# Performance work log

Measured on AMD Instinct MI355X. Metric: run time of the kernel, lower is better.

The kernel has to match this reference:

```python
import jax, jax.numpy as jnp
import numpy as np

# Model dims (match init_kwargs)
IN, H, N, W, OUT, R = 128, 512, 2048, 64, 128, 4
EPS = 1e-8


def setup_inputs() -> dict:
    key = jax.random.key(0)
    ks = jax.random.split(key, 10)
    T, B = 128, 64
    ctrl_in = IN + R * W
    s = lambda n: 1.0 / np.sqrt(n)
    return {
        "x_seq": jax.random.normal(ks[0], (T, B, IN), jnp.float32),
        "Wih": jax.random.normal(ks[1], (4 * H, ctrl_in), jnp.float32) * s(ctrl_in),
        "Whh": jax.random.normal(ks[2], (4 * H, H), jnp.float32) * s(H),
        "bih": jnp.zeros((4 * H,), jnp.float32),
        "bhh": jnp.zeros((4 * H,), jnp.float32),
        "Wout": jax.random.normal(ks[3], (OUT, H), jnp.float32) * s(H),
        "bout": jnp.zeros((OUT,), jnp.float32),
        "Wkey": jax.random.normal(ks[4], ((R + 1) * W, H), jnp.float32) * s(H),
        "bkey": jnp.zeros(((R + 1) * W,), jnp.float32),
        "alpha": jnp.float32(0.5),
        "gamma": jnp.float32(0.95),
    }


def _forward(x_seq, Wih, Whh, bih, bhh, Wout, bout, Wkey, bkey, alpha, gamma):
    T, B, _ = x_seq.shape
    h = jnp.zeros((B, H), x_seq.dtype)
    c = jnp.zeros((B, H), x_seq.dtype)
    usage = jnp.zeros((B, N), x_seq.dtype)
    read_w = jnp.zeros((B, R, N), x_seq.dtype)
    read_vec = jnp.zeros((B, R * W), x_seq.dtype)
    M = jnp.full((B, N, W), 1e-6, x_seq.dtype)  # memory reset to small const

    def step(carry, x_t):
        h, c, M, usage, read_w, read_vec = carry
        # --- LSTM controller ---
        x = jnp.concatenate([x_t, read_vec], axis=1)
        gates = x @ Wih.T + h @ Whh.T + bih + bhh  # (B, 4H)
        i, f, g, o = jnp.split(gates, 4, axis=1)
        c_new = jax.nn.sigmoid(f) * c + jax.nn.sigmoid(i) * jnp.tanh(g)
        h_new = jax.nn.sigmoid(o) * jnp.tanh(c_new)
        out = h_new @ Wout.T + bout  # (B, OUT)
        keys = (h_new @ Wkey.T + bkey).reshape(B, R + 1, W)
        read_keys = keys[:, :R]       # (B, R, W)
        write_key = keys[:, R]        # (B, W)
        # --- content-addressed read (cosine similarity + softmax over N) ---
        Mn = M / (jnp.linalg.norm(M, axis=-1, keepdims=True) + EPS)
        Kn = read_keys / (jnp.linalg.norm(read_keys, axis=-1, keepdims=True) + EPS)
        sim = jnp.einsum('brw,bnw->brn', Kn, Mn)          # (B, R, N)
        read_w_new = jax.nn.softmax(sim, axis=-1)
        read_vec_new = jnp.einsum('brn,bnw->brw', read_w_new, M).reshape(B, R * W)
        # --- LRUA write (uses PREVIOUS read/usage weights) ---
        sa = jax.nn.sigmoid(alpha)
        lu = jax.nn.one_hot(jnp.argmin(usage, axis=-1), N, dtype=M.dtype)  # (B, N)
        w_w = sa * read_w.sum(axis=1) + (1.0 - sa) * lu
        M_new = M * (1.0 - lu[:, :, None]) + w_w[:, :, None] * write_key[:, None, :]
        # --- usage update ---
        usage_new = gamma * usage + read_w_new.sum(axis=1) + w_w
        return (h_new, c_new, M_new, usage_new, read_w_new, read_vec_new), out

    _, outs = jax.lax.scan(step, (h, c, M, usage, read_w, read_vec), x_seq)
    return outs  # (T, B, OUT)


def reference(x_seq, Wih, Whh, bih, bhh, Wout, bout, Wkey, bkey, alpha, gamma):
    return _forward(x_seq, Wih, Whh, bih, bhh, Wout, bout, Wkey, bkey, alpha, gamma)
```

## Files before the change

### kernel.cpp

```cpp
#include <hip/hip_runtime.h>
#include <hip/hip_bf16.h>

#define EPSF 1e-8f

typedef __attribute__((ext_vector_type(8))) __bf16 bf8;
typedef __attribute__((ext_vector_type(4))) float f4;
typedef unsigned long long ull;

__device__ __forceinline__ short f2bf(float f) {
  union { __hip_bfloat16 b; short s; } u;
  u.b = __float2bfloat16(f);
  return u.s;
}
__device__ __forceinline__ float sigf(float x) { return 1.f / (1.f + __expf(-x)); }
__device__ __forceinline__ float red16(float v) {
  v += __shfl_xor(v, 1); v += __shfl_xor(v, 2);
  v += __shfl_xor(v, 4); v += __shfl_xor(v, 8);
  return v;
}

__device__ __forceinline__ void st_coh16(void* p, f4 v) {
  asm volatile("global_store_dwordx4 %0, %1, off sc0 sc1" :: "v"(p), "v"(v) : "memory");
}
__device__ __forceinline__ void st_coh8u(void* p, ull v) {
  asm volatile("global_store_dwordx2 %0, %1, off sc0 sc1" :: "v"(p), "v"(v) : "memory");
}
__device__ __forceinline__ void st_coh4(void* p, float v) {
  asm volatile("global_store_dword %0, %1, off sc0 sc1" :: "v"(p), "v"(v) : "memory");
}
__device__ __forceinline__ void st_coh4u(void* p, unsigned v) {
  asm volatile("global_store_dword %0, %1, off sc0 sc1" :: "v"(p), "v"(v) : "memory");
}
__device__ __forceinline__ void st_coh2(void* p, unsigned v) {
  asm volatile("global_store_short %0, %1, off sc0 sc1" :: "v"(p), "v"(v) : "memory");
}
__device__ __forceinline__ ull ald8(const void* p) {
  return __hip_atomic_load((const ull*)p, __ATOMIC_RELAXED, __HIP_MEMORY_SCOPE_AGENT);
}
__device__ __forceinline__ unsigned ald4(const void* p) {
  return __hip_atomic_load((const unsigned*)p, __ATOMIC_RELAXED, __HIP_MEMORY_SCOPE_AGENT);
}

#define LD8X4(v0,v1,v2,v3,v4,v5,v6,v7,p0,p1,p2,p3,p4,p5,p6,p7) \
  asm volatile( \
    "global_load_dwordx4 %0, %8, off sc0 sc1\n\t" \
    "global_load_dwordx4 %1, %9, off sc0 sc1\n\t" \
    "global_load_dwordx4 %2, %10, off sc0 sc1\n\t" \
    "global_load_dwordx4 %3, %11, off sc0 sc1\n\t" \
    "global_load_dwordx4 %4, %12, off sc0 sc1\n\t" \
    "global_load_dwordx4 %5, %13, off sc0 sc1\n\t" \
    "global_load_dwordx4 %6, %14, off sc0 sc1\n\t" \
    "global_load_dwordx4 %7, %15, off sc0 sc1\n\t" \
    "s_waitcnt vmcnt(0)" \
    : "=&v"(v0),"=&v"(v1),"=&v"(v2),"=&v"(v3),"=&v"(v4),"=&v"(v5),"=&v"(v6),"=&v"(v7) \
    : "v"(p0),"v"(p1),"v"(p2),"v"(p3),"v"(p4),"v"(p5),"v"(p6),"v"(p7) : "memory")

__device__ __forceinline__ void gsync(unsigned* bar, unsigned k) {
  asm volatile("s_waitcnt vmcnt(0)" ::: "memory");
  __syncthreads();
  if (threadIdx.x == 0)
    __hip_atomic_store(&bar[blockIdx.x * 16], k, __ATOMIC_RELAXED,
                       __HIP_MEMORY_SCOPE_AGENT);
  if (blockIdx.x == 255) {
    if (threadIdx.x < 64) {
      const int l = threadIdx.x;
      for (;;) {
        unsigned mn = 0xffffffffu;
#pragma unroll
        for (int j = 0; j < 4; ++j) {
          unsigned v = __hip_atomic_load(&bar[(l * 4 + j) * 16], __ATOMIC_RELAXED,
                                         __HIP_MEMORY_SCOPE_AGENT);
          mn = v < mn ? v : mn;
        }
        if (__all(mn >= k)) break;
        __builtin_amdgcn_s_sleep(1);
      }
      if (l < 8)
        __hip_atomic_store(&bar[4096 + l * 16], k, __ATOMIC_RELAXED,
                           __HIP_MEMORY_SCOPE_AGENT);
    }
  } else if (threadIdx.x == 0) {
    const unsigned g = blockIdx.x >> 5;
    while (__hip_atomic_load(&bar[4096 + g * 16], __ATOMIC_RELAXED,
                             __HIP_MEMORY_SCOPE_AGENT) < k)
      __builtin_amdgcn_s_sleep(1);
  }
  __syncthreads();
}

struct StReg { ull a, b; };

__global__ __launch_bounds__(512, 2) void mann_mega(
    const float* __restrict__ x_seq, const float* __restrict__ Wih,
    const float* __restrict__ Whh, const float* __restrict__ bih,
    const float* __restrict__ bhh, const float* __restrict__ Wout,
    const float* __restrict__ boutp, const float* __restrict__ Wkey,
    const float* __restrict__ bkeyp, const float* __restrict__ alphap,
    const float* __restrict__ gammap, float* __restrict__ out, char* ws) {
  float* rwb0 = (float*)(ws + 33554432);
  float* rwb1 = (float*)(ws + 35651584);
  float* usage = (float*)(ws + 37748736);
  float* cst = (float*)(ws + 38273024);
  short* hb0 = (short*)(ws + 38404096);
  short* hb1 = (short*)(ws + 38469632);
  float* rv0 = (float*)(ws + 38535168);
  float* rv1 = (float*)(ws + 38600704);
  float* dp = (float*)(ws + 38666240);
  float* sd0 = (float*)(ws + 38670336);
  float* sd1 = (float*)(ws + 38671360);
  unsigned* lu = (unsigned*)(ws + 38672384);
  unsigned* bar = (unsigned*)(ws + 38673408);
  short* Wc = (short*)(ws + 38693888);
  short* Wkb = (short*)(ws + 42363904);

  __shared__ float Mlds[512 * 64];
  __shared__ union {
    struct { short stage[4][2048]; } g;
    struct { float sv[512]; int si[512]; } m;
    struct { short hs[512]; float kbuf[256]; float wkbuf[64];
             float rvacc[256]; float wsum[32]; float wps[512]; } a;
  } sm;
  __shared__ float denl[256];

  const int tid = threadIdx.x;
  const int lane = tid & 63;
  const int wv = tid >> 6;
  const int s = lane & 15;
  const int q = lane >> 4;
  unsigned rnd = 0;

  {
    const unsigned gid = blockIdx.x * 512 + tid;
    const unsigned gs = 256 * 512;
    for (unsigned i4 = gid; i4 < 458752u; i4 += gs) {
      unsigned e = i4 * 4;
      unsigned row = e / 896u, k = e - row * 896u;
      float4 v = (k < 384u) ? *(const float4*)&Wih[row * 384u + k]
                            : *(const float4*)&Whh[row * 512u + (k - 384u)];
      union { short4 s4; ull u; } o;
      o.s4.x = f2bf(v.x); o.s4.y = f2bf(v.y); o.s4.z = f2bf(v.z); o.s4.w = f2bf(v.w);
      st_coh8u(Wc + e, o.u);
    }
    for (unsigned i4 = gid; i4 < 57344u; i4 += gs) {
      unsigned e = i4 * 4;
      unsigned row = e >> 9, k = e & 511u;
      float4 v = (row < 128u) ? *(const float4*)&Wout[row * 512u + k]
                              : *(const float4*)&Wkey[(row - 128u) * 512u + k];
      union { short4 s4; ull u; } o;
      o.s4.x = f2bf(v.x); o.s4.y = f2bf(v.y); o.s4.z = f2bf(v.z); o.s4.w = f2bf(v.w);
      st_coh8u(Wkb + e, o.u);
    }
    if (gid < 64u) st_coh4u(lu + gid, 0u);
  }
  gsync(bar, ++rnd);

  for (int t = 0; t < 128; ++t) {
    const int p = t & 1;
    short* hN = p ? hb1 : hb0;
    const short* hP = p ? hb0 : hb1;
    float* rwCur = p ? rwb1 : rwb0;
    const float* rwM1 = p ? rwb0 : rwb1;
    const float* rwM2 = rwCur;
    float* sdW = p ? sd1 : sd0;
    const float* sdM2 = p ? sd0 : sd1;
    float* rvW = p ? rv1 : rv0;
    const float* rvR = p ? rv0 : rv1;

    if (blockIdx.x < 64) {
      const int j0 = blockIdx.x * 8;
      if (tid < 256) {
        float iv = 1.f;
        if (t > 0) {
          union { ull u; float2 f; } a, b2;
          a.u = ald8(dp + tid * 4); b2.u = ald8(dp + tid * 4 + 2);
          iv = 1.f / (a.f.x + a.f.y + b2.f.x + b2.f.y);
        }
        denl[tid] = iv;
      }
      const int row = lane;
      const int k4 = wv;
      auto stage_load = [&](int c) -> StReg {
        StReg r; r.a = 0; r.b = 0;
        if (c < 4) {
          float4 v = *(const float4*)&x_seq[((size_t)t * 64 + row) * 128 + c * 32 + k4 * 4];
          union { float2 f; ull u; } u0, u1;
          u0.f.x = v.x; u0.f.y = v.y; u1.f.x = v.z; u1.f.y = v.w;
          r.a = u0.u; r.b = u1.u;
        } else if (c < 12) {
          if (t > 0) {
            int col = (c - 4) * 32 + k4 * 4;
            r.a = ald8(rvR + row * 256 + col);
            r.b = ald8(rvR + row * 256 + col + 2);
          }
        } else {
          if (t > 0) r.a = ald8(hP + row * 512 + (c - 12) * 32 + k4 * 4);
        }
        return r;
      };
      auto stage_store = [&](short* buf, int c, StReg r) {
        short4 o;
        if (c < 4) {
          union { ull u; float2 f; } a, b2; a.u = r.a; b2.u = r.b;
          o.x = f2bf(a.f.x); o.y = f2bf(a.f.y); o.z = f2bf(b2.f.x); o.w = f2bf(b2.f.y);
        } else if (c < 12) {
          union { ull u; float2 f; } a, b2; a.u = r.a; b2.u = r.b;
          int col = (c - 4) * 32 + k4 * 4;
          float iv = denl[row * 4 + (col >> 6)];
          o.x = f2bf(a.f.x * iv); o.y = f2bf(a.f.y * iv);
          o.z = f2bf(b2.f.x * iv); o.w = f2bf(b2.f.y * iv);
        } else {
          union { ull u; short4 s4; } a; a.u = r.a; o = a.s4;
        }
        int idx = (row >> 4) * 512 + ((row & 15) + 16 * ((k4 >> 1) & 3)) * 8 + (k4 & 1) * 4;
        *(short4*)&buf[idx] = o;
      };
      __syncthreads();
      {
        StReg r0 = stage_load(0), r1 = stage_load(1), r2 = stage_load(2);
        stage_store(sm.g.stage[0], 0, r0);
        stage_store(sm.g.stage[1], 1, r1);
        stage_store(sm.g.stage[2], 2, r2);
        StReg ra = stage_load(3);
        StReg rb = stage_load(4);
        __syncthreads();
        const int msl = wv >> 1, nh = wv & 1;
        const int rr = nh * 16 + s;
        const int gg = rr >> 3, jj = rr & 7;
        const size_t wrow = (size_t)(gg * 512 + j0 + jj) * 896;
        f4 acc = {0.f, 0.f, 0.f, 0.f};
        for (int c = 0; c < 28; ++c) {
          StReg rn;
          if (c + 5 < 28) rn = stage_load(c + 5);
          bf8 a = *(const bf8*)&sm.g.stage[c & 3][msl * 512 + lane * 8];
          bf8 bb = *(const bf8*)&Wc[wrow + c * 32 + q * 8];
          acc = __builtin_amdgcn_mfma_f32_16x16x32_bf16(a, bb, acc, 0, 0, 0);
          if (c + 3 < 28) { stage_store(sm.g.stage[(c + 3) & 3], c + 3, ra); ra = rb; rb = rn; }
          __syncthreads();
        }
        float* gbuf = (float*)sm.g.stage;
#pragma unroll
        for (int reg = 0; reg < 4; ++reg) {
          int bat = msl * 16 + q * 4 + reg;
          gbuf[bat * 33 + rr] = acc[reg];
        }
      }
      __syncthreads();
      {
        const float* gbuf = (const float*)sm.g.stage;
        int b = tid >> 3, jj = tid & 7, j = j0 + jj;
        float gi = gbuf[b * 33 + jj] + bih[j] + bhh[j];
        float gf = gbuf[b * 33 + 8 + jj] + bih[512 + j] + bhh[512 + j];
        float gg2 = gbuf[b * 33 + 16 + jj] + bih[1024 + j] + bhh[1024 + j];
        float go = gbuf[b * 33 + 24 + jj] + bih[1536 + j] + bhh[1536 + j];
        float co = (t == 0) ? 0.f : cst[b * 512 + j];
        float cn = sigf(gf) * co + sigf(gi) * tanhf(gg2);
        float hn = sigf(go) * tanhf(cn);
        cst[b * 512 + j] = cn;
        union { __hip_bfloat16 b16; unsigned short us; } hu;
        hu.b16 = __float2bfloat16(hn);
        st_coh2(hN + b * 512 + j, (unsigned)hu.us);
      }
    } else if (blockIdx.x < 128) {
      if (t > 0) {
        const int b = blockIdx.x - 64;
        f4 dp0, dp1, dp2, dp3, sm2;
        unsigned luv;
        asm volatile(
            "global_load_dwordx4 %0, %6, off sc0 sc1\n\t"
            "global_load_dwordx4 %1, %7, off sc0 sc1\n\t"
            "global_load_dwordx4 %2, %8, off sc0 sc1\n\t"
            "global_load_dwordx4 %3, %9, off sc0 sc1\n\t"
            "global_load_dwordx4 %4, %10, off sc0 sc1\n\t"
            "global_load_dword %5, %11, off sc0 sc1\n\t"
            "s_waitcnt vmcnt(0)"
            : "=&v"(dp0), "=&v"(dp1), "=&v"(dp2), "=&v"(dp3), "=&v"(sm2), "=&v"(luv)
            : "v"((const void*)(dp + (b * 4 + 0) * 4)),
              "v"((const void*)(dp + (b * 4 + 1) * 4)),
              "v"((const void*)(dp + (b * 4 + 2) * 4)),
              "v"((const void*)(dp + (b * 4 + 3) * 4)),
              "v"((const void*)(sdM2 + b * 4)), "v"((const void*)(lu + b))
            : "memory");
        float d0 = dp0.x + dp0.y + dp0.z + dp0.w;
        float d1 = dp1.x + dp1.y + dp1.z + dp1.w;
        float d2 = dp2.x + dp2.y + dp2.z + dp2.w;
        float d3 = dp3.x + dp3.y + dp3.z + dp3.w;
        if (tid == 0) { f4 dv = {d0, d1, d2, d3}; st_coh16(sdW + b * 4, dv); }
        float iC0 = 1.f / d0, iC1 = 1.f / d1, iC2 = 1.f / d2, iC3 = 1.f / d3;
        float iO0 = 0, iO1 = 0, iO2 = 0, iO3 = 0;
        if (t > 1) { iO0 = 1.f / sm2.x; iO1 = 1.f / sm2.y; iO2 = 1.f / sm2.z; iO3 = 1.f / sm2.w; }
        const float sa = sigf(alphap[0]);
        const float ga = gammap[0];
        const int luB = (int)luv;
        f4 ec[4], eo[4];
        {
          const void* pc[4]; const void* po[4];
#pragma unroll
          for (int i = 0; i < 4; ++i) {
            int n = i * 512 + tid;
            pc[i] = (const void*)(rwM1 + ((size_t)b * 2048 + n) * 4);
            po[i] = (const void*)(rwM2 + ((size_t)b * 2048 + n) * 4);
          }
          LD8X4(ec[0], ec[1], ec[2], ec[3], eo[0], eo[1], eo[2], eo[3],
                pc[0], pc[1], pc[2], pc[3], po[0], po[1], po[2], po[3]);
        }
        float vm = INFINITY;
        int im = 0x7fffffff;
#pragma unroll
        for (int i = 0; i < 4; ++i) {
          int n = i * 512 + tid;
          float wps = (t > 1) ? (eo[i].x * iO0 + eo[i].y * iO1 + eo[i].z * iO2 + eo[i].w * iO3)
                              : 0.f;
          float ww = sa * wps + (1.f - sa) * ((n == luB) ? 1.f : 0.f);
          float sn = ec[i].x * iC0 + ec[i].y * iC1 + ec[i].z * iC2 + ec[i].w * iC3;
          float uo = (t == 1) ? 0.f : usage[b * 2048 + n];
          float u = ga * uo + sn + ww;
          usage[b * 2048 + n] = u;
          if (u < vm) { vm = u; im = n; }
        }
        sm.m.sv[tid] = vm; sm.m.si[tid] = im;
        __syncthreads();
        for (int off = 256; off > 0; off >>= 1) {
          if (tid < off) {
            float v2 = sm.m.sv[tid + off]; int j2 = sm.m.si[tid + off];
            if (v2 < sm.m.sv[tid] || (v2 == sm.m.sv[tid] && j2 < sm.m.si[tid])) {
              sm.m.sv[tid] = v2; sm.m.si[tid] = j2;
            }
          }
          __syncthreads();
        }
        if (tid == 0) st_coh4u(lu + b, (unsigned)sm.m.si[0]);
      }
    } else if (blockIdx.x < 192) {
      const int bz = blockIdx.x - 128;
      if (tid < 64) { f4 z = {0, 0, 0, 0}; st_coh16(rvW + bz * 256 + tid * 4, z); }
    }
    gsync(bar, ++rnd);

    {
      const int b = blockIdx.x >> 2, ch = blockIdx.x & 3;
      if (tid < 128) {
        union { ull u; uint2 v; } hv;
        hv.u = ald8(hN + b * 512 + tid * 4);
        *(uint2*)&sm.a.hs[tid * 4] = hv.v;
      }
      if (tid < 256) sm.a.rvacc[tid] = 0.f;
      unsigned luv = 0;
      if (t > 0) {
        luv = ald4(lu + b);
        union { ull u; float2 f; } s0, s1, e0, e1;
        s0.u = ald8(sdW + b * 4); s1.u = ald8(sdW + b * 4 + 2);
        const size_t eb = ((size_t)b * 2048 + ch * 512 + tid) * 4;
        e0.u = ald8(rwM1 + eb); e1.u = ald8(rwM1 + eb + 2);
        sm.a.wps[tid] = e0.f.x / s0.f.x + e0.f.y / s0.f.y +
                        e1.f.x / s1.f.x + e1.f.y / s1.f.y;
      } else {
        sm.a.wps[tid] = 0.f;
      }
      __syncthreads();
      for (int pp = 0; pp < 11; ++pp) {
        int idx = pp * 32 + wv * 4 + q;
        int wr; float bias;
        if (idx < 320) { wr = 128 + idx; bias = bkeyp[idx]; }
        else { wr = ch * 32 + (idx - 320); bias = boutp[wr]; }
        float acc = 0.f;
#pragma unroll
        for (int i = 0; i < 4; ++i) {
          bf8 w8 = *(const bf8*)&Wkb[(size_t)wr * 512 + i * 128 + s * 8];
          bf8 h8 = *(const bf8*)&sm.a.hs[i * 128 + s * 8];
#pragma unroll
          for (int j = 0; j < 8; ++j) acc += (float)w8[j] * (float)h8[j];
        }
        acc = red16(acc) + bias;
        if (s == 0) {
          if (idx < 256) sm.a.kbuf[idx] = acc;
          else if (idx < 320) sm.a.wkbuf[idx - 256] = acc;
          else out[((size_t)t * 64 + b) * 128 + wr] = acc;
        }
      }
      __syncthreads();
      float4 kn[4];
#pragma unroll
      for (int r = 0; r < 4; ++r) {
        float4 k4 = *(float4*)&sm.a.kbuf[r * 64 + s * 4];
        float ss = k4.x * k4.x + k4.y * k4.y + k4.z * k4.z + k4.w * k4.w;
        ss = red16(ss);
        float iv = 1.f / (sqrtf(ss) + EPSF);
        kn[r].x = k4.x * iv; kn[r].y = k4.y * iv;
        kn[r].z = k4.z * iv; kn[r].w = k4.w * iv;
      }
      const float4 wk = *(float4*)&sm.a.wkbuf[s * 4];
      const float sa = sigf(alphap[0]);
      const int luB = (int)luv;
      float4 rva0 = {0,0,0,0}, rva1 = {0,0,0,0}, rva2 = {0,0,0,0}, rva3 = {0,0,0,0};
      float es0 = 0.f, es1 = 0.f, es2 = 0.f, es3 = 0.f;
      for (int i = 0; i < 16; ++i) {
        const int nl = wv * 64 + i * 4 + q;
        const int n = ch * 512 + nl;
        float4 m4;
        if (t > 0) m4 = *(float4*)&Mlds[nl * 64 + s * 4];
        else { m4.x = 1e-6f; m4.y = 1e-6f; m4.z = 1e-6f; m4.w = 1e-6f; }
        float ssm = m4.x * m4.x + m4.y * m4.y + m4.z * m4.z + m4.w * m4.w;
        float d0 = m4.x * kn[0].x + m4.y * kn[0].y + m4.z * kn[0].z + m4.w * kn[0].w;
        float d1 = m4.x * kn[1].x + m4.y * kn[1].y + m4.z * kn[1].z + m4.w * kn[1].w;
        float d2 = m4.x * kn[2].x + m4.y * kn[2].y + m4.z * kn[2].z + m4.w * kn[2].w;
        float d3 = m4.x * kn[3].x + m4.y * kn[3].y + m4.z * kn[3].z + m4.w * kn[3].w;
        ssm = red16(ssm);
        d0 = red16(d0); d1 = red16(d1); d2 = red16(d2); d3 = red16(d3);
        float iv = 1.f / (sqrtf(ssm) + EPSF);
        float e0 = __expf(d0 * iv), e1 = __expf(d1 * iv);
        float e2 = __expf(d2 * iv), e3 = __expf(d3 * iv);
        rva0.x += e0 * m4.x; rva0.y += e0 * m4.y; rva0.z += e0 * m4.z; rva0.w += e0 * m4.w;
        rva1.x += e1 * m4.x; rva1.y += e1 * m4.y; rva1.z += e1 * m4.z; rva1.w += e1 * m4.w;
        rva2.x += e2 * m4.x; rva2.y += e2 * m4.y; rva2.z += e2 * m4.z; rva2.w += e2 * m4.w;
        rva3.x += e3 * m4.x; rva3.y += e3 * m4.y; rva3.z += e3 * m4.z; rva3.w += e3 * m4.w;
        if (s == 0) {
          f4 ev = {e0, e1, e2, e3};
          st_coh16(rwCur + ((size_t)b * 2048 + n) * 4, ev);
          es0 += e0; es1 += e1; es2 += e2; es3 += e3;
        }
        float wps = sm.a.wps[nl];
        float onehot = (n == luB) ? 1.f : 0.f;
        float ww = sa * wps + (1.f - sa) * onehot;
        float keep = 1.f - onehot;
        float4 mn;
        mn.x = m4.x * keep + ww * wk.x;
        mn.y = m4.y * keep + ww * wk.y;
        mn.z = m4.z * keep + ww * wk.z;
        mn.w = m4.w * keep + ww * wk.w;
        *(float4*)&Mlds[nl * 64 + s * 4] = mn;
      }
      es0 += __shfl_xor(es0, 16); es0 += __shfl_xor(es0, 32);
      es1 += __shfl_xor(es1, 16); es1 += __shfl_xor(es1, 32);
      es2 += __shfl_xor(es2, 16); es2 += __shfl_xor(es2, 32);
      es3 += __shfl_xor(es3, 16); es3 += __shfl_xor(es3, 32);
      if (lane == 0) {
        sm.a.wsum[wv * 4 + 0] = es0; sm.a.wsum[wv * 4 + 1] = es1;
        sm.a.wsum[wv * 4 + 2] = es2; sm.a.wsum[wv * 4 + 3] = es3;
      }
#define REDQ(v) { v += __shfl_xor(v, 16); v += __shfl_xor(v, 32); }
      REDQ(rva0.x) REDQ(rva0.y) REDQ(rva0.z) REDQ(rva0.w)
      REDQ(rva1.x) REDQ(rva1.y) REDQ(rva1.z) REDQ(rva1.w)
      REDQ(rva2.x) REDQ(rva2.y) REDQ(rva2.z) REDQ(rva2.w)
      REDQ(rva3.x) REDQ(rva3.y) REDQ(rva3.z) REDQ(rva3.w)
#undef REDQ
      if (q == 0) {
        atomicAdd(&sm.a.rvacc[0 * 64 + s * 4 + 0], rva0.x);
        atomicAdd(&sm.a.rvacc[0 * 64 + s * 4 + 1], rva0.y);
        atomicAdd(&sm.a.rvacc[0 * 64 + s * 4 + 2], rva0.z);
        atomicAdd(&sm.a.rvacc[0 * 64 + s * 4 + 3], rva0.w);
        atomicAdd(&sm.a.rvacc[1 * 64 + s * 4 + 0], rva1.x);
        atomicAdd(&sm.a.rvacc[1 * 64 + s * 4 + 1], rva1.y);
        atomicAdd(&sm.a.rvacc[1 * 64 + s * 4 + 2], rva1.z);
        atomicAdd(&sm.a.rvacc[1 * 64 + s * 4 + 3], rva1.w);
        atomicAdd(&sm.a.rvacc[2 * 64 + s * 4 + 0], rva2.x);
        atomicAdd(&sm.a.rvacc[2 * 64 + s * 4 + 1], rva2.y);
        atomicAdd(&sm.a.rvacc[2 * 64 + s * 4 + 2], rva2.z);
        atomicAdd(&sm.a.rvacc[2 * 64 + s * 4 + 3], rva2.w);
        atomicAdd(&sm.a.rvacc[3 * 64 + s * 4 + 0], rva3.x);
        atomicAdd(&sm.a.rvacc[3 * 64 + s * 4 + 1], rva3.y);
        atomicAdd(&sm.a.rvacc[3 * 64 + s * 4 + 2], rva3.z);
        atomicAdd(&sm.a.rvacc[3 * 64 + s * 4 + 3], rva3.w);
      }
      __syncthreads();
      if (tid < 4) {
        float ssum = 0.f;
        for (int w8 = 0; w8 < 8; ++w8) ssum += sm.a.wsum[w8 * 4 + tid];
        st_coh4(dp + (b * 4 + tid) * 4 + ch, ssum);
      }
      if (tid < 256) {
        float v = sm.a.rvacc[tid];
        atomicAdd(rvW + b * 256 + tid, v);
      }
    }
    gsync(bar, ++rnd);
  }
}

extern "C" void kernel_launch(void* const* d_in, const int* in_sizes, int n_in,
                              void* d_out, int out_size, void* d_ws, size_t ws_size,
                              hipStream_t stream) {
  const float* x_seq = (const float*)d_in[0];
  const float* Wih = (const float*)d_in[1];
  const float* Whh = (const float*)d_in[2];
  const float* bih = (const float*)d_in[3];
  const float* bhh = (const float*)d_in[4];
  const float* Wout = (const float*)d_in[5];
  const float* bout = (const float*)d_in[6];
  const float* Wkey = (const float*)d_in[7];
  const float* bkey = (const float*)d_in[8];
  const float* alpha = (const float*)d_in[9];
  const float* gamma = (const float*)d_in[10];
  float* out = (float*)d_out;
  char* ws = (char*)d_ws;

  hipMemsetAsync(ws + 38673408, 0, 20480, stream);
  mann_mega<<<256, 512, 0, stream>>>(x_seq, Wih, Whh, bih, bhh, Wout, bout,
                                     Wkey, bkey, alpha, gamma, out, ws);
}
```

Measured before the change: 5.678 ms.

## Prefetch all gate staging loads upfront and use LDS-only barriers

The LSTM gate blocks now issue all 28 staging global loads into registers before the MFMA loop, instead of a rolling 5-deep prefetch. This exposes every global load latency at once and keeps four LDS stages in flight. Several __syncthreads are also replaced by a barrier that waits only on LDS counters (lgkmcnt), so outstanding global loads no longer drain at each barrier. The cost is much higher register pressure, and the partial wait could be unsafe if any barrier-protected data came from a pending global access.

Result: no change. 5.650 ms (-0.5%).

```diff
diff --git a/kernel.cpp b/kernel.cpp
--- a/kernel.cpp
+++ b/kernel.cpp
@@ -6,6 +6,9 @@
 typedef __attribute__((ext_vector_type(8))) __bf16 bf8;
 typedef __attribute__((ext_vector_type(4))) float f4;
 typedef unsigned long long ull;
+
+#define LBAR() do { asm volatile("s_waitcnt lgkmcnt(0)" ::: "memory"); \
+                    __builtin_amdgcn_s_barrier(); } while (0)
 
 __device__ __forceinline__ short f2bf(float f) {
   union { __hip_bfloat16 b; short s; } u;
@@ -214,29 +217,28 @@
         int idx = (row >> 4) * 512 + ((row & 15) + 16 * ((k4 >> 1) & 3)) * 8 + (k4 & 1) * 4;
         *(short4*)&buf[idx] = o;
       };
+      StReg regs[28];
+#pragma unroll
+      for (int c = 0; c < 28; ++c) regs[c] = stage_load(c);
       __syncthreads();
+#pragma unroll
+      for (int c = 0; c < 4; ++c) stage_store(sm.g.stage[c], c, regs[c]);
+      LBAR();
       {
-        StReg r0 = stage_load(0), r1 = stage_load(1), r2 = stage_load(2);
-        stage_store(sm.g.stage[0], 0, r0);
-        stage_store(sm.g.stage[1], 1, r1);
-        stage_store(sm.g.stage[2], 2, r2);
-        StReg ra = stage_load(3);
-        StReg rb = stage_load(4);
-        __syncthreads();
         const int msl = wv >> 1, nh = wv & 1;
         const int rr = nh * 16 + s;
         const int gg = rr >> 3, jj = rr & 7;
         const size_t wrow = (size_t)(gg * 512 + j0 + jj) * 896;
         f4 acc = {0.f, 0.f, 0.f, 0.f};
+#pragma unroll
         for (int c = 0; c < 28; ++c) {
-          StReg rn;
-          if (c + 5 < 28) rn = stage_load(c + 5);
           bf8 a = *(const bf8*)&sm.g.stage[c & 3][msl * 512 + lane * 8];
           bf8 bb = *(const bf8*)&Wc[wrow + c * 32 + q * 8];
           acc = __builtin_amdgcn_mfma_f32_16x16x32_bf16(a, bb, acc, 0, 0, 0);
-          if (c + 3 < 28) { stage_store(sm.g.stage[(c + 3) & 3], c + 3, ra); ra = rb; rb = rn; }
-          __syncthreads();
-        }
+          LBAR();
+          if (c + 4 < 28) stage_store(sm.g.stage[(c + 4) & 3], c + 4, regs[c + 4]);
+        }
+        LBAR();
         float* gbuf = (float*)sm.g.stage;
 #pragma unroll
         for (int reg = 0; reg < 4; ++reg) {
@@ -244,7 +246,7 @@
           gbuf[bat * 33 + rr] = acc[reg];
         }
       }
-      __syncthreads();
+      LBAR();
       {
         const float* gbuf = (const float*)sm.g.stage;
         int b = tid >> 3, jj = tid & 7, j = j0 + jj;
@@ -318,7 +320,7 @@
           if (u < vm) { vm = u; im = n; }
         }
         sm.m.sv[tid] = vm; sm.m.si[tid] = im;
-        __syncthreads();
+        LBAR();
         for (int off = 256; off > 0; off >>= 1) {
           if (tid < off) {
             float v2 = sm.m.sv[tid + off]; int j2 = sm.m.si[tid + off];
@@ -326,7 +328,7 @@
               sm.m.sv[tid] = v2; sm.m.si[tid] = j2;
             }
           }
-          __syncthreads();
+          LBAR();
         }
         if (tid == 0) st_coh4u(lu + b, (unsigned)sm.m.si[0]);
       }
@@ -377,7 +379,7 @@
           else out[((size_t)t * 64 + b) * 128 + wr] = acc;
         }
       }
-      __syncthreads();
+      LBAR();
       float4 kn[4];
 #pragma unroll
       for (int r = 0; r < 4; ++r) {
@@ -461,7 +463,7 @@
         atomicAdd(&sm.a.rvacc[3 * 64 + s * 4 + 2], rva3.z);
         atomicAdd(&sm.a.rvacc[3 * 64 + s * 4 + 3], rva3.w);
       }
-      __syncthreads();
+      LBAR();
       if (tid < 4) {
         float ssum = 0.f;
         for (int w8 = 0; w8 < 8; ++w8) ssum += sm.a.wsum[w8 * 4 + tid];
```
